# Performance work log

Hardware: AMD Instinct MI355X
Metric: run time of the kernel (lower is better)

## Reference

```python
import jax, jax.numpy as jnp
import numpy as np

B, N, D = 8, 4096, 128
P, K = 256, 64            # n_patches, n_pts_per_patch (= FoldingNet num_fine)
DFF, GRID = 1024, 2
G2 = GRID * GRID
NC = K // G2              # num_coarse
EPS = 1e-5                # BatchNorm eps (eval mode, running stats)


def fps(xyz, n):
    """Farthest point sampling on one cloud xyz [N,3] -> n int32 indices."""
    Np = xyz.shape[0]
    def step(carry, _):
        mind, last = carry
        d = jnp.sum((xyz - xyz[last]) ** 2, -1)
        mind = jnp.minimum(mind, d)
        nxt = jnp.argmax(mind).astype(jnp.int32)
        return (mind, nxt), nxt
    (_, _), idx = jax.lax.scan(step, (jnp.full((Np,), 1e10, xyz.dtype), jnp.int32(0)), None, length=n - 1)
    return jnp.concatenate([jnp.zeros((1,), jnp.int32), idx])


def setup_inputs() -> dict:
    key = jax.random.key(0)
    ks = jax.random.split(key, 24)
    rn = lambda i, s, sc=1.0: sc * jax.random.normal(ks[i], s, dtype=jnp.float32)
    inp = {
        'xyz': rn(0, (B, N, 3)),
        'feat': rn(1, (B, N, D)),
        # FoldingNet.xyz_mlp (Linear weights stored [in,out])
        'w1': rn(2, (D, DFF), 0.09), 'b1': rn(3, (DFF,), 0.02),
        'w2': rn(4, (DFF, DFF), 0.03), 'b2': rn(5, (DFF,), 0.02),
        'w3': rn(6, (DFF, 3 * NC), 0.03), 'b3': rn(7, (3 * NC,), 0.02),
        # FoldingNet.final_conv (1x1 conv weights stored [in,out]), BN eval stats
        'cw1': rn(8, (D + 5, DFF), 0.09), 'cb1': rn(9, (DFF,), 0.02),
        'g1': 0.5 + jax.random.uniform(ks[10], (DFF,), dtype=jnp.float32),
        'be1': rn(11, (DFF,), 0.02), 'm1': rn(12, (DFF,), 0.1),
        'v1': 0.5 + jax.random.uniform(ks[13], (DFF,), dtype=jnp.float32),
        'cw2': rn(14, (DFF, DFF), 0.03), 'cb2': rn(15, (DFF,), 0.02),
        'g2': 0.5 + jax.random.uniform(ks[16], (DFF,), dtype=jnp.float32),
        'be2': rn(17, (DFF,), 0.02), 'm2': rn(18, (DFF,), 0.1),
        'v2': 0.5 + jax.random.uniform(ks[19], (DFF,), dtype=jnp.float32),
        'cw3': rn(20, (DFF, 3), 0.03), 'cb3': rn(21, (3,), 0.02),
    }
    return inp


def reference(xyz, feat, w1, b1, w2, b2, w3, b3,
              cw1, cb1, g1, be1, m1, v1,
              cw2, cb2, g2, be2, m2, v2, cw3, cb3):
    # ---- point_forward: FPS -> square_distance -> masked topk -> gather -> maxpool ----
    fidx = jax.vmap(lambda p: fps(p, P))(xyz)                          # [B,P]
    patch_xyz = jnp.take_along_axis(xyz, fidx[:, :, None], 1)          # [B,P,3]
    d = (jnp.sum(xyz ** 2, -1)[:, :, None]
         + jnp.sum(patch_xyz ** 2, -1)[:, None, :]
         - 2.0 * jnp.einsum('bnc,bpc->bnp', xyz, patch_xyz))           # [B,N,P]
    # equal-sized dense batches => to_dense_batch mask is all-true (no 1e10 fill needed)
    _, gidx = jax.lax.top_k(-jnp.swapaxes(d, 1, 2), K)                 # [B,P,K] nearest
    bidx = jnp.arange(B)[:, None, None]
    grouped_feat = feat[bidx, gidx]                                    # [B,P,K,D]
    patch_feat = jnp.max(grouped_feat, axis=-2)                        # [B,P,D]
    grouped_xyz_norm = xyz[bidx, gidx] - patch_xyz[:, :, None, :]      # [B,P,K,3]

    # ---- FoldingNet decoder ----
    pf = patch_feat.reshape(B * P, D)
    h = jax.nn.relu(pf @ w1 + b1)
    h = jax.nn.relu(h @ w2 + b2)
    coarse = (h @ w3 + b3).reshape(B * P, NC, 3)                       # [BP,NC,3]
    pts = jnp.repeat(coarse, G2, axis=1)                               # [BP,K,3] (center)
    a = jnp.linspace(-0.05, 0.05, GRID, dtype=pf.dtype)
    seed2 = jnp.stack([jnp.tile(a, GRID), jnp.repeat(a, GRID)], -1)    # [G2,2]
    seedf = jnp.tile(seed2, (NC, 1))                                   # [K,2]
    featc = jnp.concatenate([
        jnp.broadcast_to(pf[:, None, :], (B * P, K, D)),
        jnp.broadcast_to(seedf[None], (B * P, K, 2)),
        pts], axis=-1)                                                 # [BP,K,D+5]
    bn = lambda x, g, be, m, v: (x - m) * (g * jax.lax.rsqrt(v + EPS)) + be
    h1 = jax.nn.relu(bn(featc @ cw1 + cb1, g1, be1, m1, v1))
    h2 = jax.nn.relu(bn(h1 @ cw2 + cb2, g2, be2, m2, v2))
    fine = h2 @ cw3 + cb3 + pts                                        # [BP,K,3]

    # ---- Chamfer L2 (mean(dist1)+mean(dist2)) between fine and grouped points ----
    gxyz = grouped_xyz_norm.reshape(B * P, K, 3)
    dd = jnp.sum((fine[:, :, None, :] - gxyz[:, None, :, :]) ** 2, -1) # [BP,K,K]
    loss_recon = jnp.mean(jnp.min(dd, axis=2)) + jnp.mean(jnp.min(dd, axis=1))
    return loss_recon
```

## Files before the change

### kernel.cpp

```cpp
#include <hip/hip_runtime.h>
#include <hip/hip_bf16.h>
#include <stdint.h>

#define DEV __device__ __forceinline__

using bf16x8  = __attribute__((ext_vector_type(8))) __bf16;
using floatx4 = __attribute__((ext_vector_type(4))) float;
using int32x8 = __attribute__((ext_vector_type(8))) int;

constexpr int Bb  = 8;
constexpr int Nn  = 4096;
constexpr int Dd  = 128;
constexpr int Pp  = 256;
constexpr int Kk  = 64;
constexpr int BP  = Bb * Pp;
constexpr int M2  = BP * Kk;
constexpr float EPSBN = 1e-5f;

DEV unsigned short f2bf(float f) {
  uint32_t u = __float_as_uint(f);
  u += 0x7fffu + ((u >> 16) & 1u);
  return (unsigned short)(u >> 16);
}
DEV float bf2f(unsigned short h) { return __uint_as_float(((uint32_t)h) << 16); }

DEV void async_copy16(const void* g, const void* l) {
  __builtin_amdgcn_global_load_lds(
      (__attribute__((address_space(1))) uint32_t*)(uintptr_t)g,
      (__attribute__((address_space(3))) uint32_t*)(uint32_t)(uintptr_t)l,
      16, 0, 0);
}

__global__ void prep_k(const float* g1, const float* be1, const float* m1, const float* v1, const float* cb1,
                       const float* g2, const float* be2, const float* m2, const float* v2, const float* cb2,
                       float* sc1, float* sh1, float* sc2, float* sh2, float* out) {
  int t = threadIdx.x;
  float s1 = g1[t] * rsqrtf(v1[t] + EPSBN);
  sc1[t] = s1; sh1[t] = (cb1[t] - m1[t]) * s1 + be1[t];
  float s2 = g2[t] * rsqrtf(v2[t] + EPSBN);
  sc2[t] = s2; sh2[t] = (cb2[t] - m2[t]) * s2 + be2[t];
  if (t == 0) out[0] = 0.f;
}

__global__ void cvt16(const float* __restrict__ in, unsigned short* __restrict__ out, int Kd, int Nd) {
  __shared__ float ts[32][33];
  int tx = threadIdx.x & 31, ty = threadIdx.x >> 5;
  int n0 = blockIdx.x * 32, k0 = blockIdx.y * 32;
#pragma unroll
  for (int r = 0; r < 4; ++r)
    ts[ty + 8 * r][tx] = in[(size_t)(k0 + ty + 8 * r) * Nd + n0 + tx];
  __syncthreads();
#pragma unroll
  for (int r = 0; r < 4; ++r)
    out[(size_t)(n0 + ty + 8 * r) * Kd + k0 + tx] = f2bf(ts[tx][ty + 8 * r]);
}

__global__ void cvt8(const float* __restrict__ in, uint8_t* __restrict__ out, int Kd, int Nd) {
  __shared__ float ts[32][33];
  int tx = threadIdx.x & 31, ty = threadIdx.x >> 5;
  int n0 = blockIdx.x * 32, k0 = blockIdx.y * 32;
#pragma unroll
  for (int r = 0; r < 4; ++r)
    ts[ty + 8 * r][tx] = in[(size_t)(k0 + ty + 8 * r) * Nd + n0 + tx];
  __syncthreads();
#pragma unroll
  for (int r = 0; r < 4; ++r) {
    float v = ts[tx][ty + 8 * r];
    int w = __builtin_amdgcn_cvt_pk_fp8_f32(v, v, 0, false);
    out[(size_t)(n0 + ty + 8 * r) * Kd + k0 + tx] = (uint8_t)(w & 0xff);
  }
}

#define DPPF(v, CTRL) __uint_as_float((uint32_t)__builtin_amdgcn_update_dpp( \
    (int)__float_as_uint(v), (int)__float_as_uint(v), CTRL, 0xF, 0xF, false))
#define DPPI(v, CTRL) __builtin_amdgcn_update_dpp(v, v, CTRL, 0xF, 0xF, false)
#define RSTEP2(CTRL) { \
    float od = DPPF(bv, CTRL); \
    int oi = DPPI(bi, CTRL); \
    bool tk = (od > bv) || (od == bv && oi < bi); \
    bv = tk ? od : bv; bi = tk ? oi : bi; }

__global__ __launch_bounds__(256)
void fps_k(const float* __restrict__ xyz, float* __restrict__ pxyz) {
  int b = blockIdx.x, tid = threadIdx.x;
  int lane = tid & 63, wv = tid >> 6;
  __shared__ float xs[Nn], ys[Nn], zs[Nn];
  __shared__ uint64_t cand[2][4];
  float xr[16], yr[16], zr[16], md[16];
#pragma unroll
  for (int j = 0; j < 16; ++j) {
    int i = tid + j * 256;
    const float* q = &xyz[(size_t)(b * Nn + i) * 3];
    float x = q[0], y = q[1], z = q[2];
    xr[j] = x; yr[j] = y; zr[j] = z; md[j] = 1e10f;
    xs[i] = x; ys[i] = y; zs[i] = z;
  }
  __syncthreads();
  const float* q0 = &xyz[(size_t)(b * Nn) * 3];
  float lx = q0[0], ly = q0[1], lz = q0[2];
  if (tid == 0) {
    pxyz[(size_t)(b * Pp) * 3 + 0] = lx;
    pxyz[(size_t)(b * Pp) * 3 + 1] = ly;
    pxyz[(size_t)(b * Pp) * 3 + 2] = lz;
  }
  for (int p = 1; p < Pp; ++p) {
    float bv = -1.f; int bi = 0x7fffffff;
#pragma unroll
    for (int j = 0; j < 16; ++j) {
      float dx = __fadd_rn(xr[j], -lx);
      float dy = __fadd_rn(yr[j], -ly);
      float dz = __fadd_rn(zr[j], -lz);
      float d = __fadd_rn(__fadd_rn(__fmul_rn(dx, dx), __fmul_rn(dy, dy)), __fmul_rn(dz, dz));
      float m = fminf(md[j], d);
      md[j] = m;
      if (m > bv) { bv = m; bi = tid + j * 256; }
    }
    RSTEP2(0x111) RSTEP2(0x112) RSTEP2(0x114) RSTEP2(0x118) RSTEP2(0x142) RSTEP2(0x143)
    int s = p & 1;
    if (lane == 63)
      cand[s][wv] = ((uint64_t)(uint32_t)__float_as_uint(bv) << 32) |
                    (uint32_t)(0x7fffffff - bi);
    __syncthreads();
    uint64_t k0 = cand[s][0], k1 = cand[s][1], k2 = cand[s][2], k3 = cand[s][3];
    uint64_t ka = (k0 > k1) ? k0 : k1;
    uint64_t kb = (k2 > k3) ? k2 : k3;
    uint64_t kw = (ka > kb) ? ka : kb;
    int wi = 0x7fffffff - (int)(uint32_t)(kw & 0xffffffffu);
    lx = xs[wi]; ly = ys[wi]; lz = zs[wi];
    if (tid == 0) {
      pxyz[(size_t)(b * Pp + p) * 3 + 0] = lx;
      pxyz[(size_t)(b * Pp + p) * 3 + 1] = ly;
      pxyz[(size_t)(b * Pp + p) * 3 + 2] = lz;
    }
  }
}

__global__ __launch_bounds__(256)
void group_k(const float* __restrict__ xyz, const float* __restrict__ feat,
             const float* __restrict__ pxyz, unsigned short* __restrict__ pfb,
             float* __restrict__ gxyz) {
  int bp = blockIdx.x, tid = threadIdx.x;
  int b = bp >> 8;
  __shared__ uint32_t dbits[Nn];
  __shared__ uint32_t hist[256];
  __shared__ int sel[64];
  __shared__ uint32_t svDigit, svWant, svClt, svCeq;
  __shared__ float red[256];
  float px = pxyz[(size_t)bp * 3], py = pxyz[(size_t)bp * 3 + 1], pz = pxyz[(size_t)bp * 3 + 2];
  for (int i = tid; i < Nn; i += 256) {
    const float* q = &xyz[(size_t)(b * Nn + i) * 3];
    float dx = q[0] - px, dy = q[1] - py, dz = q[2] - pz;
    dbits[i] = __float_as_uint(dx * dx + dy * dy + dz * dz);
  }
  uint32_t prefix = 0, want = 64;
  for (int shift = 24; shift >= 0; shift -= 8) {
    __syncthreads();
    hist[tid] = 0;
    __syncthreads();
    for (int i = tid; i < Nn; i += 256) {
      uint32_t v = dbits[i];
      bool match = (shift == 24) || ((v >> (shift + 8)) == prefix);
      if (match) atomicAdd(&hist[(v >> shift) & 255], 1u);
    }
    __syncthreads();
    uint32_t myh = hist[tid];
    for (int off = 1; off < 256; off <<= 1) {
      uint32_t o = (tid >= off) ? hist[tid - off] : 0u;
      __syncthreads();
      hist[tid] += o;
      __syncthreads();
    }
    uint32_t cum = hist[tid];
    uint32_t prev = cum - myh;
    if (prev < want && want <= cum) { svDigit = (uint32_t)tid; svWant = want - prev; }
    __syncthreads();
    prefix = (prefix << 8) | svDigit;
    want = svWant;
  }
  uint32_t tval = prefix;
  if (tid == 0) { svClt = 0; svCeq = 0; }
  __syncthreads();
  for (int i = tid; i < Nn; i += 256) {
    if (dbits[i] < tval) { uint32_t pos = atomicAdd(&svClt, 1u); sel[pos] = i; }
  }
  __syncthreads();
  uint32_t clt = svClt;
  for (int i = tid; i < Nn; i += 256) {
    if (dbits[i] == tval) {
      uint32_t pos = atomicAdd(&svCeq, 1u);
      if (clt + pos < 64) sel[clt + pos] = i;
    }
  }
  __syncthreads();
  if (tid < 192) {
    int k = tid / 3, c = tid - k * 3;
    float sub = (c == 0) ? px : (c == 1) ? py : pz;
    gxyz[(size_t)bp * 192 + tid] = xyz[(size_t)(b * Nn + sel[k]) * 3 + c] - sub;
  }
  int dch = tid & 127, half = tid >> 7;
  float m = -1e30f;
  for (int k = half * 32; k < half * 32 + 32; ++k)
    m = fmaxf(m, feat[(size_t)(b * Nn + sel[k]) * Dd + dch]);
  red[tid] = m;
  __syncthreads();
  if (half == 0) pfb[(size_t)bp * Dd + dch] = f2bf(fmaxf(m, red[tid + 128]));
}

template <int EPI>
__global__ __launch_bounds__(256)
void gemm_bt(const unsigned short* __restrict__ A, const unsigned short* __restrict__ Bt,
             float* __restrict__ Cf, unsigned short* __restrict__ Ch,
             const float* __restrict__ p0,
             int Npar, int Kd, int nbn) {
  __shared__ __align__(16) unsigned short As[128 * 32];
  __shared__ __align__(16) unsigned short Bs[128 * 32];
  const int tid = threadIdx.x;
  const int lane = tid & 63, wid = tid >> 6;
  const int bn = blockIdx.x % nbn, bm = blockIdx.x / nbn;
  const int m0 = bm * 128, n0 = bn * 128;
  const int quad = lane >> 4, l15 = lane & 15;
  const int wm = wid & 1, wn = wid >> 1;

  floatx4 acc[4][4];
#pragma unroll
  for (int i = 0; i < 4; ++i)
#pragma unroll
    for (int j = 0; j < 4; ++j) acc[i][j] = floatx4{0.f, 0.f, 0.f, 0.f};

  const int c0i = tid, c1i = tid + 256;
  const int r0 = c0i >> 2, o0 = (c0i & 3) * 8;
  const int r1 = c1i >> 2, o1 = (c1i & 3) * 8;

  for (int k0 = 0; k0 < Kd; k0 += 32) {
    async_copy16(A + (size_t)(m0 + r0) * Kd + k0 + o0, &As[c0i * 8]);
    async_copy16(A + (size_t)(m0 + r1) * Kd + k0 + o1, &As[c1i * 8]);
    async_copy16(Bt + (size_t)(n0 + r0) * Kd + k0 + o0, &Bs[c0i * 8]);
    async_copy16(Bt + (size_t)(n0 + r1) * Kd + k0 + o1, &Bs[c1i * 8]);
    __syncthreads();
    const bf16x8* Ap = reinterpret_cast<const bf16x8*>(As);
    const bf16x8* Bp = reinterpret_cast<const bf16x8*>(Bs);
    bf16x8 af[4], bfv[4];
#pragma unroll
    for (int t = 0; t < 4; ++t) {
      af[t]  = Ap[(wm * 64 + t * 16 + l15) * 4 + quad];
      bfv[t] = Bp[(wn * 64 + t * 16 + l15) * 4 + quad];
    }
#pragma unroll
    for (int mt = 0; mt < 4; ++mt)
#pragma unroll
      for (int nt = 0; nt < 4; ++nt)
        acc[mt][nt] = __builtin_amdgcn_mfma_f32_16x16x32_bf16(af[mt], bfv[nt], acc[mt][nt], 0, 0, 0);
    __syncthreads();
  }

  const int rowBase = m0 + wm * 64 + quad * 4;
  const int colBase = n0 + wn * 64 + l15;

  if (EPI == 0) {
#pragma unroll
    for (int mt = 0; mt < 4; ++mt)
#pragma unroll
      for (int nt = 0; nt < 4; ++nt)
#pragma unroll
        for (int r = 0; r < 4; ++r)
          Cf[(size_t)(rowBase + mt * 16 + r) * Npar + colBase + nt * 16] = acc[mt][nt][r];
  } else {
#pragma unroll
    for (int nt = 0; nt < 4; ++nt) {
      float bias = p0[colBase + nt * 16];
#pragma unroll
      for (int mt = 0; mt < 4; ++mt)
#pragma unroll
        for (int r = 0; r < 4; ++r) {
          float v = fmaxf(acc[mt][nt][r] + bias, 0.f);
          Ch[(size_t)(rowBase + mt * 16 + r) * Npar + colBase + nt * 16] = f2bf(v);
        }
    }
  }
}

__global__ __launch_bounds__(256)
void gemm_mx3(const uint8_t* __restrict__ A, const uint8_t* __restrict__ Bt,
              const float* __restrict__ p0, const float* __restrict__ p1,
              const float* __restrict__ cw3, const float* __restrict__ coarse,
              const float* __restrict__ cb3, float* __restrict__ fine,
              int rowOff, int Kd) {
  __shared__ __align__(128) uint8_t As[128 * 128];
  __shared__ __align__(128) uint8_t Bs[128 * 128];
  __shared__ float fsum[2][2][64][3];
  const int tid = threadIdx.x;
  const int lane = tid & 63, wid = tid >> 6;
  const int bm = blockIdx.x;
  const int m0 = bm * 128;
  const int quad = lane >> 4, l15 = lane & 15;
  const int wm = wid & 1, wn = wid >> 1;

  float fp[4][4][3];
#pragma unroll
  for (int mt = 0; mt < 4; ++mt)
#pragma unroll
    for (int r = 0; r < 4; ++r)
      fp[mt][r][0] = fp[mt][r][1] = fp[mt][r][2] = 0.f;

  for (int bn = 0; bn < 8; ++bn) {
    const int n0 = bn * 128;
    floatx4 acc[4][4];
#pragma unroll
    for (int i = 0; i < 4; ++i)
#pragma unroll
      for (int j = 0; j < 4; ++j) acc[i][j] = floatx4{0.f, 0.f, 0.f, 0.f};

    for (int k0 = 0; k0 < Kd; k0 += 128) {
#pragma unroll
      for (int c = 0; c < 4; ++c) {
        int ci = c * 256 + tid;
        int row = ci >> 3, cp = ci & 7;
        int cc = cp ^ (row & 7);
        async_copy16(A + (size_t)(m0 + row) * Kd + k0 + cc * 16, &As[ci * 16]);
        async_copy16(Bt + (size_t)(n0 + row) * Kd + k0 + cc * 16, &Bs[ci * 16]);
      }
      __syncthreads();
      const uint4* Ap = (const uint4*)As;
      const uint4* Bp = (const uint4*)Bs;
      int32x8 av[4], bv[4];
#pragma unroll
      for (int t = 0; t < 4; ++t) {
        int rm = wm * 64 + t * 16 + l15;
        int rn = wn * 64 + t * 16 + l15;
        int swm = rm & 7, swn = rn & 7;
        uint4 alo = Ap[rm * 8 + ((2 * quad) ^ swm)];
        uint4 ahi = Ap[rm * 8 + ((2 * quad + 1) ^ swm)];
        uint4 blo = Bp[rn * 8 + ((2 * quad) ^ swn)];
        uint4 bhi = Bp[rn * 8 + ((2 * quad + 1) ^ swn)];
        av[t] = int32x8{(int)alo.x, (int)alo.y, (int)alo.z, (int)alo.w,
                        (int)ahi.x, (int)ahi.y, (int)ahi.z, (int)ahi.w};
        bv[t] = int32x8{(int)blo.x, (int)blo.y, (int)blo.z, (int)blo.w,
                        (int)bhi.x, (int)bhi.y, (int)bhi.z, (int)bhi.w};
      }
#pragma unroll
      for (int mt = 0; mt < 4; ++mt)
#pragma unroll
        for (int nt = 0; nt < 4; ++nt)
          acc[mt][nt] = __builtin_amdgcn_mfma_scale_f32_16x16x128_f8f6f4(
              av[mt], bv[nt], acc[mt][nt], 0, 0, 0, 127, 0, 127);
      __syncthreads();
    }

    const int colBase = n0 + wn * 64 + l15;
#pragma unroll
    for (int nt = 0; nt < 4; ++nt) {
      int col = colBase + nt * 16;
      float sc = p0[col], sh = p1[col];
      float c0 = cw3[col * 3], c1 = cw3[col * 3 + 1], c2 = cw3[col * 3 + 2];
#pragma unroll
      for (int mt = 0; mt < 4; ++mt)
#pragma unroll
        for (int r = 0; r < 4; ++r) {
          float v = fmaxf(acc[mt][nt][r] * sc + sh, 0.f);
          fp[mt][r][0] += v * c0; fp[mt][r][1] += v * c1; fp[mt][r][2] += v * c2;
        }
    }
  }

#pragma unroll
  for (int off = 1; off < 16; off <<= 1)
#pragma unroll
    for (int mt = 0; mt < 4; ++mt)
#pragma unroll
      for (int r = 0; r < 4; ++r)
#pragma unroll
        for (int i = 0; i < 3; ++i)
          fp[mt][r][i] += __shfl_xor(fp[mt][r][i], off, 64);
  if (l15 == 0) {
#pragma unroll
    for (int mt = 0; mt < 4; ++mt)
#pragma unroll
      for (int r = 0; r < 4; ++r) {
        int rowLocal = quad * 4 + mt * 16 + r;
#pragma unroll
        for (int i = 0; i < 3; ++i) fsum[wm][wn][rowLocal][i] = fp[mt][r][i];
      }
  }
  __syncthreads();
  for (int t = tid; t < 128 * 3; t += 256) {
    int row = t / 3, i = t - row * 3;
    float s = fsum[row >> 6][0][row & 63][i] + fsum[row >> 6][1][row & 63][i];
    int g = rowOff + m0 + row;
    int bp = g >> 6, kp = g & 63, j = kp >> 2;
    fine[(size_t)g * 3 + i] = s + cb3[i] + coarse[(size_t)bp * 48 + j * 3 + i];
  }
}

__global__ __launch_bounds__(256)
void coarse_k(const unsigned short* __restrict__ h2m, const float* __restrict__ w3,
              const float* __restrict__ b3, float* __restrict__ coarse) {
  int r = blockIdx.x, tid = threadIdx.x;
  __shared__ float hrow[1024];
  __shared__ float part[192];
  for (int i = tid; i < 1024; i += 256) hrow[i] = bf2f(h2m[(size_t)r * 1024 + i]);
  __syncthreads();
  if (tid < 192) {
    int j = tid % 48, seg = tid / 48;
    float acc = 0.f;
    for (int k = seg * 256; k < seg * 256 + 256; ++k) acc += hrow[k] * w3[(size_t)k * 48 + j];
    part[tid] = acc;
  }
  __syncthreads();
  if (tid < 48)
    coarse[(size_t)r * 48 + tid] = part[tid] + part[tid + 48] + part[tid + 96] + part[tid + 144] + b3[tid];
}

__global__ __launch_bounds__(256)
void h1build_k(const float* __restrict__ u1, const float* __restrict__ cw1,
               const float* __restrict__ coarse, const float* __restrict__ sc1,
               const float* __restrict__ sh1, uint8_t* __restrict__ h1) {
  int bp = blockIdx.x, tid = threadIdx.x;
  __shared__ float co[48];
  if (tid < 48) co[tid] = coarse[(size_t)bp * 48 + tid];
  __syncthreads();
  int n0 = tid * 4;
  float4 un  = *(const float4*)&u1[(size_t)bp * 1024 + n0];
  float4 a0  = *(const float4*)&cw1[128 * 1024 + n0];
  float4 a1  = *(const float4*)&cw1[129 * 1024 + n0];
  float4 b0  = *(const float4*)&cw1[130 * 1024 + n0];
  float4 b1v = *(const float4*)&cw1[131 * 1024 + n0];
  float4 b2v = *(const float4*)&cw1[132 * 1024 + n0];
  float4 sc  = *(const float4*)&sc1[n0];
  float4 sh  = *(const float4*)&sh1[n0];
  const float sxv[4] = {-0.05f, 0.05f, -0.05f, 0.05f};
  const float syv[4] = {-0.05f, -0.05f, 0.05f, 0.05f};
  float s[4][4];
#pragma unroll
  for (int g = 0; g < 4; ++g) {
    s[g][0] = sxv[g] * a0.x + syv[g] * a1.x;
    s[g][1] = sxv[g] * a0.y + syv[g] * a1.y;
    s[g][2] = sxv[g] * a0.z + syv[g] * a1.z;
    s[g][3] = sxv[g] * a0.w + syv[g] * a1.w;
  }
  uint32_t* out = (uint32_t*)h1;
  for (int k = 0; k < 64; ++k) {
    int j = k >> 2, g = k & 3;
    float c0 = co[j * 3], c1 = co[j * 3 + 1], c2 = co[j * 3 + 2];
    float x0 = un.x + s[g][0] + c0 * b0.x + c1 * b1v.x + c2 * b2v.x;
    float x1 = un.y + s[g][1] + c0 * b0.y + c1 * b1v.y + c2 * b2v.y;
    float x2 = un.z + s[g][2] + c0 * b0.z + c1 * b1v.z + c2 * b2v.z;
    float x3 = un.w + s[g][3] + c0 * b0.w + c1 * b1v.w + c2 * b2v.w;
    float v0 = fmaxf(x0 * sc.x + sh.x, 0.f);
    float v1 = fmaxf(x1 * sc.y + sh.y, 0.f);
    float v2 = fmaxf(x2 * sc.z + sh.z, 0.f);
    float v3 = fmaxf(x3 * sc.w + sh.w, 0.f);
    int w = __builtin_amdgcn_cvt_pk_fp8_f32(v0, v1, 0, false);
    w = __builtin_amdgcn_cvt_pk_fp8_f32(v2, v3, w, true);
    out[(size_t)(bp * 64 + k) * 256 + tid] = (uint32_t)w;
  }
}

__global__ __launch_bounds__(256)
void chamfer_k(const float* __restrict__ fine, const float* __restrict__ gxyz,
               float* __restrict__ out) {
  int tid = threadIdx.x, wv = tid >> 6, lane = tid & 63;
  int bp = blockIdx.x * 4 + wv;
  __shared__ float sf[4][64][3], sg[4][64][3];
  const float* fr = &fine[(size_t)(bp * 64 + lane) * 3];
  const float* gr = &gxyz[(size_t)(bp * 64 + lane) * 3];
  sf[wv][lane][0] = fr[0]; sf[wv][lane][1] = fr[1]; sf[wv][lane][2] = fr[2];
  sg[wv][lane][0] = gr[0]; sg[wv][lane][1] = gr[1]; sg[wv][lane][2] = gr[2];
  __syncthreads();
  float f0 = sf[wv][lane][0], f1 = sf[wv][lane][1], f2 = sf[wv][lane][2];
  float g0 = sg[wv][lane][0], g1 = sg[wv][lane][1], g2 = sg[wv][lane][2];
  float rmin = 1e30f, cmin = 1e30f;
  for (int j = 0; j < 64; ++j) {
    float dx = f0 - sg[wv][j][0], dy = f1 - sg[wv][j][1], dz = f2 - sg[wv][j][2];
    rmin = fminf(rmin, dx * dx + dy * dy + dz * dz);
    float ex = sf[wv][j][0] - g0, ey = sf[wv][j][1] - g1, ez = sf[wv][j][2] - g2;
    cmin = fminf(cmin, ex * ex + ey * ey + ez * ez);
  }
  float tot = rmin + cmin;
  for (int off = 32; off; off >>= 1) tot += __shfl_down(tot, off, 64);
  if (lane == 0) atomicAdd(out, tot * (1.0f / 131072.0f));
}

extern "C" void kernel_launch(void* const* d_in, const int* in_sizes, int n_in,
                              void* d_out, int out_size, void* d_ws, size_t ws_size,
                              hipStream_t stream) {
  (void)in_sizes; (void)n_in; (void)out_size;
  const float* xyz = (const float*)d_in[0];
  const float* feat = (const float*)d_in[1];
  const float* w1 = (const float*)d_in[2];
  const float* b1 = (const float*)d_in[3];
  const float* w2 = (const float*)d_in[4];
  const float* b2 = (const float*)d_in[5];
  const float* w3 = (const float*)d_in[6];
  const float* b3 = (const float*)d_in[7];
  const float* cw1 = (const float*)d_in[8];
  const float* cb1 = (const float*)d_in[9];
  const float* g1 = (const float*)d_in[10];
  const float* be1 = (const float*)d_in[11];
  const float* m1 = (const float*)d_in[12];
  const float* v1 = (const float*)d_in[13];
  const float* cw2 = (const float*)d_in[14];
  const float* cb2 = (const float*)d_in[15];
  const float* g2 = (const float*)d_in[16];
  const float* be2 = (const float*)d_in[17];
  const float* m2 = (const float*)d_in[18];
  const float* v2 = (const float*)d_in[19];
  const float* cw3 = (const float*)d_in[20];
  const float* cb3 = (const float*)d_in[21];
  float* out = (float*)d_out;

  uint8_t* ws = (uint8_t*)d_ws;
  size_t off = 0;
  auto alloc = [&](size_t bytes) {
    void* p = ws + off;
    off = (off + bytes + 255) & ~(size_t)255;
    return p;
  };
  float*          pxyz  = (float*)alloc((size_t)BP * 3 * 4);
  unsigned short* w1t   = (unsigned short*)alloc((size_t)1024 * 128 * 2);
  unsigned short* cw1t  = (unsigned short*)alloc((size_t)1024 * 128 * 2);
  unsigned short* w2t   = (unsigned short*)alloc((size_t)1024 * 1024 * 2);
  uint8_t*        cw2t8 = (uint8_t*)alloc((size_t)1024 * 1024);
  float*          sc1   = (float*)alloc(4096);
  float*          sh1   = (float*)alloc(4096);
  float*          sc2   = (float*)alloc(4096);
  float*          sh2   = (float*)alloc(4096);
  unsigned short* pfb   = (unsigned short*)alloc((size_t)BP * 128 * 2);
  float*          gxyz  = (float*)alloc((size_t)BP * 64 * 3 * 4);
  float*          u1    = (float*)alloc((size_t)BP * 1024 * 4);
  unsigned short* hb    = (unsigned short*)alloc((size_t)BP * 1024 * 2);
  unsigned short* h2m   = (unsigned short*)alloc((size_t)BP * 1024 * 2);
  float*          coarse = (float*)alloc((size_t)BP * 48 * 4);
  float*          fine  = (float*)alloc((size_t)M2 * 3 * 4);

  size_t perPatch = (size_t)Kk * 1024;
  size_t avail = (ws_size > off) ? (ws_size - off - 256) : 0;
  int ppc = 2;
  while (ppc < BP && (size_t)(ppc * 2) * perPatch <= avail) ppc *= 2;
  uint8_t* h1 = (uint8_t*)alloc((size_t)ppc * perPatch);
  int nch = BP / ppc;

  prep_k<<<1, 1024, 0, stream>>>(g1, be1, m1, v1, cb1, g2, be2, m2, v2, cb2,
                                 sc1, sh1, sc2, sh2, out);
  cvt16<<<dim3(1024 / 32, 128 / 32), 256, 0, stream>>>(w1, w1t, 128, 1024);
  cvt16<<<dim3(1024 / 32, 128 / 32), 256, 0, stream>>>(cw1, cw1t, 128, 1024);
  cvt16<<<dim3(1024 / 32, 1024 / 32), 256, 0, stream>>>(w2, w2t, 1024, 1024);
  cvt8<<<dim3(1024 / 32, 1024 / 32), 256, 0, stream>>>(cw2, cw2t8, 1024, 1024);
  fps_k<<<Bb, 256, 0, stream>>>(xyz, pxyz);
  group_k<<<BP, 256, 0, stream>>>(xyz, feat, pxyz, pfb, gxyz);
  gemm_bt<0><<<(2048 / 128) * 8, 256, 0, stream>>>(pfb, cw1t, u1, nullptr, nullptr,
                                                   1024, 128, 8);
  gemm_bt<1><<<(2048 / 128) * 8, 256, 0, stream>>>(pfb, w1t, nullptr, hb, b1,
                                                   1024, 128, 8);
  gemm_bt<1><<<(2048 / 128) * 8, 256, 0, stream>>>(hb, w2t, nullptr, h2m, b2,
                                                   1024, 1024, 8);
  coarse_k<<<2048, 256, 0, stream>>>(h2m, w3, b3, coarse);
  for (int c = 0; c < nch; ++c) {
    int pstart = c * ppc;
    int nbm = ppc * Kk / 128;
    h1build_k<<<ppc, 256, 0, stream>>>(u1 + (size_t)pstart * 1024, cw1,
                                       coarse + (size_t)pstart * 48, sc1, sh1, h1);
    gemm_mx3<<<nbm, 256, 0, stream>>>(
        h1, cw2t8, sc2, sh2, cw3, coarse, cb3, fine, pstart * Kk, 1024);
  }
  chamfer_k<<<BP / 4, 256, 0, stream>>>(fine, gxyz, out);
}
```

Baseline: 645.9 us.

## Fuse h1 construction into FP8 GEMM, build A tile in shared memory

Moves the h1build computation (rank-5 update of u1 plus BN and ReLU, then FP8 packing) into the gemm_mx3 prologue. Each block now builds a 32-row by 1024-col FP8 A tile directly in LDS instead of reading h1 from a global workspace. This removes the chunked h1 round trip through global memory and the per-chunk launch loop, replacing them with one launch of M2/32 blocks. In exchange the M tile shrinks from 128 to 32 rows, so each block reloads the whole B weight matrix for less output work, which raises weight traffic and lowers MFMA reuse per B load.

```diff
diff --git a/kernel.cpp b/kernel.cpp
--- a/kernel.cpp
+++ b/kernel.cpp
@@ -280,113 +280,139 @@
 }
 
 __global__ __launch_bounds__(256)
-void gemm_mx3(const uint8_t* __restrict__ A, const uint8_t* __restrict__ Bt,
+void gemm_mx3(const float* __restrict__ u1, const float* __restrict__ cw1,
+              const float* __restrict__ coarse, const float* __restrict__ sc1,
+              const float* __restrict__ sh1,
+              const uint8_t* __restrict__ Bt,
               const float* __restrict__ p0, const float* __restrict__ p1,
-              const float* __restrict__ cw3, const float* __restrict__ coarse,
-              const float* __restrict__ cb3, float* __restrict__ fine,
-              int rowOff, int Kd) {
-  __shared__ __align__(128) uint8_t As[128 * 128];
+              const float* __restrict__ cw3, const float* __restrict__ cb3,
+              float* __restrict__ fine) {
+  __shared__ __align__(128) uint8_t As[32 * 1024];
   __shared__ __align__(128) uint8_t Bs[128 * 128];
-  __shared__ float fsum[2][2][64][3];
+  __shared__ float fsum[2][2][16][3];
   const int tid = threadIdx.x;
   const int lane = tid & 63, wid = tid >> 6;
   const int bm = blockIdx.x;
-  const int m0 = bm * 128;
   const int quad = lane >> 4, l15 = lane & 15;
   const int wm = wid & 1, wn = wid >> 1;
-
-  float fp[4][4][3];
-#pragma unroll
-  for (int mt = 0; mt < 4; ++mt)
-#pragma unroll
-    for (int r = 0; r < 4; ++r)
-      fp[mt][r][0] = fp[mt][r][1] = fp[mt][r][2] = 0.f;
+  const int bp = bm >> 1;
+
+  {
+    int n0c = tid * 4;
+    float4 un  = *(const float4*)&u1[(size_t)bp * 1024 + n0c];
+    float4 a0  = *(const float4*)&cw1[128 * 1024 + n0c];
+    float4 a1  = *(const float4*)&cw1[129 * 1024 + n0c];
+    float4 b0  = *(const float4*)&cw1[130 * 1024 + n0c];
+    float4 b1v = *(const float4*)&cw1[131 * 1024 + n0c];
+    float4 b2v = *(const float4*)&cw1[132 * 1024 + n0c];
+    float4 sc  = *(const float4*)&sc1[n0c];
+    float4 sh  = *(const float4*)&sh1[n0c];
+    const float sxv[4] = {-0.05f, 0.05f, -0.05f, 0.05f};
+    const float syv[4] = {-0.05f, -0.05f, 0.05f, 0.05f};
+    uint32_t* Aw = (uint32_t*)As;
+    int gc = tid >> 2;
+    int dw = tid & 3;
+    for (int row = 0; row < 32; ++row) {
+      int gi = row & 3;
+      int j = (bm & 1) * 8 + (row >> 2);
+      float c0 = coarse[(size_t)bp * 48 + j * 3 + 0];
+      float c1 = coarse[(size_t)bp * 48 + j * 3 + 1];
+      float c2 = coarse[(size_t)bp * 48 + j * 3 + 2];
+      float sx = sxv[gi], sy = syv[gi];
+      float x0 = un.x + sx * a0.x + sy * a1.x + c0 * b0.x + c1 * b1v.x + c2 * b2v.x;
+      float x1 = un.y + sx * a0.y + sy * a1.y + c0 * b0.y + c1 * b1v.y + c2 * b2v.y;
+      float x2 = un.z + sx * a0.z + sy * a1.z + c0 * b0.z + c1 * b1v.z + c2 * b2v.z;
+      float x3 = un.w + sx * a0.w + sy * a1.w + c0 * b0.w + c1 * b1v.w + c2 * b2v.w;
+      float v0 = fmaxf(x0 * sc.x + sh.x, 0.f);
+      float v1 = fmaxf(x1 * sc.y + sh.y, 0.f);
+      float v2 = fmaxf(x2 * sc.z + sh.z, 0.f);
+      float v3 = fmaxf(x3 * sc.w + sh.w, 0.f);
+      int w = __builtin_amdgcn_cvt_pk_fp8_f32(v0, v1, 0, false);
+      w = __builtin_amdgcn_cvt_pk_fp8_f32(v2, v3, w, true);
+      int phys = (gc & ~7) | ((gc & 7) ^ (row & 7));
+      Aw[row * 256 + phys * 4 + dw] = (uint32_t)w;
+    }
+  }
+  float fp[4][3];
+#pragma unroll
+  for (int r = 0; r < 4; ++r) fp[r][0] = fp[r][1] = fp[r][2] = 0.f;
+  __syncthreads();
+
+  const uint4* Ap = (const uint4*)As;
+  const int rm = wm * 16 + l15;
+  const int swm = rm & 7;
 
   for (int bn = 0; bn < 8; ++bn) {
     const int n0 = bn * 128;
-    floatx4 acc[4][4];
-#pragma unroll
-    for (int i = 0; i < 4; ++i)
-#pragma unroll
-      for (int j = 0; j < 4; ++j) acc[i][j] = floatx4{0.f, 0.f, 0.f, 0.f};
-
-    for (int k0 = 0; k0 < Kd; k0 += 128) {
+    floatx4 acc[4];
+#pragma unroll
+    for (int j = 0; j < 4; ++j) acc[j] = floatx4{0.f, 0.f, 0.f, 0.f};
+
+    for (int k0 = 0; k0 < 1024; k0 += 128) {
 #pragma unroll
       for (int c = 0; c < 4; ++c) {
         int ci = c * 256 + tid;
         int row = ci >> 3, cp = ci & 7;
         int cc = cp ^ (row & 7);
-        async_copy16(A + (size_t)(m0 + row) * Kd + k0 + cc * 16, &As[ci * 16]);
-        async_copy16(Bt + (size_t)(n0 + row) * Kd + k0 + cc * 16, &Bs[ci * 16]);
+        async_copy16(Bt + (size_t)(n0 + row) * 1024 + k0 + cc * 16, &Bs[ci * 16]);
       }
       __syncthreads();
-      const uint4* Ap = (const uint4*)As;
       const uint4* Bp = (const uint4*)Bs;
-      int32x8 av[4], bv[4];
-#pragma unroll
-      for (int t = 0; t < 4; ++t) {
-        int rm = wm * 64 + t * 16 + l15;
-        int rn = wn * 64 + t * 16 + l15;
-        int swm = rm & 7, swn = rn & 7;
-        uint4 alo = Ap[rm * 8 + ((2 * quad) ^ swm)];
-        uint4 ahi = Ap[rm * 8 + ((2 * quad + 1) ^ swm)];
+      int kc = k0 >> 4;
+      uint4 alo = Ap[rm * 64 + kc + ((2 * quad) ^ swm)];
+      uint4 ahi = Ap[rm * 64 + kc + ((2 * quad + 1) ^ swm)];
+      int32x8 av = int32x8{(int)alo.x, (int)alo.y, (int)alo.z, (int)alo.w,
+                           (int)ahi.x, (int)ahi.y, (int)ahi.z, (int)ahi.w};
+      int32x8 bv[4];
+#pragma unroll
+      for (int nt = 0; nt < 4; ++nt) {
+        int rn = wn * 64 + nt * 16 + l15;
+        int swn = rn & 7;
         uint4 blo = Bp[rn * 8 + ((2 * quad) ^ swn)];
         uint4 bhi = Bp[rn * 8 + ((2 * quad + 1) ^ swn)];
-        av[t] = int32x8{(int)alo.x, (int)alo.y, (int)alo.z, (int)alo.w,
-                        (int)ahi.x, (int)ahi.y, (int)ahi.z, (int)ahi.w};
-        bv[t] = int32x8{(int)blo.x, (int)blo.y, (int)blo.z, (int)blo.w,
-                        (int)bhi.x, (int)bhi.y, (int)bhi.z, (int)bhi.w};
+        bv[nt] = int32x8{(int)blo.x, (int)blo.y, (int)blo.z, (int)blo.w,
+                         (int)bhi.x, (int)bhi.y, (int)bhi.z, (int)bhi.w};
       }
 #pragma unroll
-      for (int mt = 0; mt < 4; ++mt)
-#pragma unroll
-        for (int nt = 0; nt < 4; ++nt)
-          acc[mt][nt] = __builtin_amdgcn_mfma_scale_f32_16x16x128_f8f6f4(
-              av[mt], bv[nt], acc[mt][nt], 0, 0, 0, 127, 0, 127);
+      for (int nt = 0; nt < 4; ++nt)
+        acc[nt] = __builtin_amdgcn_mfma_scale_f32_16x16x128_f8f6f4(
+            av, bv[nt], acc[nt], 0, 0, 0, 127, 0, 127);
       __syncthreads();
     }
 
-    const int colBase = n0 + wn * 64 + l15;
 #pragma unroll
     for (int nt = 0; nt < 4; ++nt) {
-      int col = colBase + nt * 16;
+      int col = n0 + wn * 64 + nt * 16 + l15;
       float sc = p0[col], sh = p1[col];
       float c0 = cw3[col * 3], c1 = cw3[col * 3 + 1], c2 = cw3[col * 3 + 2];
 #pragma unroll
-      for (int mt = 0; mt < 4; ++mt)
-#pragma unroll
-        for (int r = 0; r < 4; ++r) {
-          float v = fmaxf(acc[mt][nt][r] * sc + sh, 0.f);
-          fp[mt][r][0] += v * c0; fp[mt][r][1] += v * c1; fp[mt][r][2] += v * c2;
-        }
+      for (int r = 0; r < 4; ++r) {
+        float v = fmaxf(acc[nt][r] * sc + sh, 0.f);
+        fp[r][0] += v * c0; fp[r][1] += v * c1; fp[r][2] += v * c2;
+      }
     }
   }
 
 #pragma unroll
   for (int off = 1; off < 16; off <<= 1)
 #pragma unroll
-    for (int mt = 0; mt < 4; ++mt)
-#pragma unroll
-      for (int r = 0; r < 4; ++r)
-#pragma unroll
-        for (int i = 0; i < 3; ++i)
-          fp[mt][r][i] += __shfl_xor(fp[mt][r][i], off, 64);
+    for (int r = 0; r < 4; ++r)
+#pragma unroll
+      for (int i = 0; i < 3; ++i)
+        fp[r][i] += __shfl_xor(fp[r][i], off, 64);
   if (l15 == 0) {
 #pragma unroll
-    for (int mt = 0; mt < 4; ++mt)
-#pragma unroll
-      for (int r = 0; r < 4; ++r) {
-        int rowLocal = quad * 4 + mt * 16 + r;
-#pragma unroll
-        for (int i = 0; i < 3; ++i) fsum[wm][wn][rowLocal][i] = fp[mt][r][i];
-      }
-  }
-  __syncthreads();
-  for (int t = tid; t < 128 * 3; t += 256) {
-    int row = t / 3, i = t - row * 3;
-    float s = fsum[row >> 6][0][row & 63][i] + fsum[row >> 6][1][row & 63][i];
-    int g = rowOff + m0 + row;
-    int bp = g >> 6, kp = g & 63, j = kp >> 2;
+    for (int r = 0; r < 4; ++r)
+#pragma unroll
+      for (int i = 0; i < 3; ++i)
+        fsum[wm][wn][quad * 4 + r][i] = fp[r][i];
+  }
+  __syncthreads();
+  if (tid < 96) {
+    int row = tid / 3, i = tid - row * 3;
+    float s = fsum[row >> 4][0][row & 15][i] + fsum[row >> 4][1][row & 15][i];
+    int g = bm * 32 + row;
+    int j = (bm & 1) * 8 + ((row & 31) >> 2);
     fine[(size_t)g * 3 + i] = s + cb3[i] + coarse[(size_t)bp * 48 + j * 3 + i];
   }
 }
@@ -408,51 +434,6 @@
   __syncthreads();
   if (tid < 48)
     coarse[(size_t)r * 48 + tid] = part[tid] + part[tid + 48] + part[tid + 96] + part[tid + 144] + b3[tid];
-}
-
-__global__ __launch_bounds__(256)
-void h1build_k(const float* __restrict__ u1, const float* __restrict__ cw1,
-               const float* __restrict__ coarse, const float* __restrict__ sc1,
-               const float* __restrict__ sh1, uint8_t* __restrict__ h1) {
-  int bp = blockIdx.x, tid = threadIdx.x;
-  __shared__ float co[48];
-  if (tid < 48) co[tid] = coarse[(size_t)bp * 48 + tid];
-  __syncthreads();
-  int n0 = tid * 4;
-  float4 un  = *(const float4*)&u1[(size_t)bp * 1024 + n0];
-  float4 a0  = *(const float4*)&cw1[128 * 1024 + n0];
-  float4 a1  = *(const float4*)&cw1[129 * 1024 + n0];
-  float4 b0  = *(const float4*)&cw1[130 * 1024 + n0];
-  float4 b1v = *(const float4*)&cw1[131 * 1024 + n0];
-  float4 b2v = *(const float4*)&cw1[132 * 1024 + n0];
-  float4 sc  = *(const float4*)&sc1[n0];
-  float4 sh  = *(const float4*)&sh1[n0];
-  const float sxv[4] = {-0.05f, 0.05f, -0.05f, 0.05f};
-  const float syv[4] = {-0.05f, -0.05f, 0.05f, 0.05f};
-  float s[4][4];
-#pragma unroll
-  for (int g = 0; g < 4; ++g) {
-    s[g][0] = sxv[g] * a0.x + syv[g] * a1.x;
-    s[g][1] = sxv[g] * a0.y + syv[g] * a1.y;
-    s[g][2] = sxv[g] * a0.z + syv[g] * a1.z;
-    s[g][3] = sxv[g] * a0.w + syv[g] * a1.w;
-  }
-  uint32_t* out = (uint32_t*)h1;
-  for (int k = 0; k < 64; ++k) {
-    int j = k >> 2, g = k & 3;
-    float c0 = co[j * 3], c1 = co[j * 3 + 1], c2 = co[j * 3 + 2];
-    float x0 = un.x + s[g][0] + c0 * b0.x + c1 * b1v.x + c2 * b2v.x;
-    float x1 = un.y + s[g][1] + c0 * b0.y + c1 * b1v.y + c2 * b2v.y;
-    float x2 = un.z + s[g][2] + c0 * b0.z + c1 * b1v.z + c2 * b2v.z;
-    float x3 = un.w + s[g][3] + c0 * b0.w + c1 * b1v.w + c2 * b2v.w;
-    float v0 = fmaxf(x0 * sc.x + sh.x, 0.f);
-    float v1 = fmaxf(x1 * sc.y + sh.y, 0.f);
-    float v2 = fmaxf(x2 * sc.z + sh.z, 0.f);
-    float v3 = fmaxf(x3 * sc.w + sh.w, 0.f);
-    int w = __builtin_amdgcn_cvt_pk_fp8_f32(v0, v1, 0, false);
-    w = __builtin_amdgcn_cvt_pk_fp8_f32(v2, v3, w, true);
-    out[(size_t)(bp * 64 + k) * 256 + tid] = (uint32_t)w;
-  }
 }
 
 __global__ __launch_bounds__(256)
@@ -483,7 +464,7 @@
 extern "C" void kernel_launch(void* const* d_in, const int* in_sizes, int n_in,
                               void* d_out, int out_size, void* d_ws, size_t ws_size,
                               hipStream_t stream) {
-  (void)in_sizes; (void)n_in; (void)out_size;
+  (void)in_sizes; (void)n_in; (void)out_size; (void)ws_size;
   const float* xyz = (const float*)d_in[0];
   const float* feat = (const float*)d_in[1];
   const float* w1 = (const float*)d_in[2];
@@ -532,13 +513,6 @@
   float*          coarse = (float*)alloc((size_t)BP * 48 * 4);
   float*          fine  = (float*)alloc((size_t)M2 * 3 * 4);
 
-  size_t perPatch = (size_t)Kk * 1024;
-  size_t avail = (ws_size > off) ? (ws_size - off - 256) : 0;
-  int ppc = 2;
-  while (ppc < BP && (size_t)(ppc * 2) * perPatch <= avail) ppc *= 2;
-  uint8_t* h1 = (uint8_t*)alloc((size_t)ppc * perPatch);
-  int nch = BP / ppc;
-
   prep_k<<<1, 1024, 0, stream>>>(g1, be1, m1, v1, cb1, g2, be2, m2, v2, cb2,
                                  sc1, sh1, sc2, sh2, out);
   cvt16<<<dim3(1024 / 32, 128 / 32), 256, 0, stream>>>(w1, w1t, 128, 1024);
@@ -554,13 +528,7 @@
   gemm_bt<1><<<(2048 / 128) * 8, 256, 0, stream>>>(hb, w2t, nullptr, h2m, b2,
                                                    1024, 1024, 8);
   coarse_k<<<2048, 256, 0, stream>>>(h2m, w3, b3, coarse);
-  for (int c = 0; c < nch; ++c) {
-    int pstart = c * ppc;
-    int nbm = ppc * Kk / 128;
-    h1build_k<<<ppc, 256, 0, stream>>>(u1 + (size_t)pstart * 1024, cw1,
-                                       coarse + (size_t)pstart * 48, sc1, sh1, h1);
-    gemm_mx3<<<nbm, 256, 0, stream>>>(
-        h1, cw2t8, sc2, sh2, cw3, coarse, cb3, fine, pstart * Kk, 1024);
-  }
+  gemm_mx3<<<M2 / 32, 256, 0, stream>>>(u1, cw1, coarse, sc1, sh1,
+                                        cw2t8, sc2, sh2, cw3, cb3, fine);
   chamfer_k<<<BP / 4, 256, 0, stream>>>(fine, gxyz, out);
 }
```

Result: slower. 691.0 us (+7.0%).
